# Kernel optimization log

Hardware: AMD Instinct MI355X
Metric: run time of the kernel (lower is better)

The kernel has to match this reference:

```python
import jax, jax.numpy as jnp
import numpy as np

B, S, E, H = 2, 2048, 2048, 16
D = E // H  # head_dim = 128


def setup_inputs() -> dict:
    key = jax.random.key(0)
    ks = jax.random.split(key, 7)
    x = jax.random.normal(ks[0], (B, S, E), dtype=jnp.float32)
    cos = jax.random.uniform(ks[1], (S, D), dtype=jnp.float32)
    sin = jax.random.uniform(ks[2], (S, D), dtype=jnp.float32)
    scale = 1.0 / np.sqrt(E)
    Wq = jax.random.normal(ks[3], (E, E), dtype=jnp.float32) * scale
    Wk = jax.random.normal(ks[4], (E, E), dtype=jnp.float32) * scale
    Wv = jax.random.normal(ks[5], (E, E), dtype=jnp.float32) * scale
    Wo = jax.random.normal(ks[6], (E, E), dtype=jnp.float32) * scale
    return {"x": x, "cos": cos, "sin": sin, "Wq": Wq, "Wk": Wk, "Wv": Wv, "Wo": Wo}


def _apply_rope(t, cos, sin):
    # t: [B, S, H, D]; cos/sin: [S, D]. NeoX rotate-half.
    half = t.shape[-1] // 2
    rotate = jnp.concatenate([-t[..., half:], t[..., :half]], axis=-1)
    return t * cos[None, :, None, :] + rotate * sin[None, :, None, :]


def reference(x, cos, sin, Wq, Wk, Wv, Wo):
    b, s, e = x.shape
    q = (x @ Wq.T).reshape(b, s, H, D)
    k = (x @ Wk.T).reshape(b, s, H, D)
    v = (x @ Wv.T).reshape(b, s, H, D)
    q = _apply_rope(q, cos, sin).transpose(0, 2, 1, 3)  # [B,H,S,D]
    k = _apply_rope(k, cos, sin).transpose(0, 2, 1, 3)
    v = v.transpose(0, 2, 1, 3)
    scale = 1.0 / jnp.sqrt(jnp.asarray(D, dtype=x.dtype))
    scores = jnp.einsum("bhqd,bhkd->bhqk", q, k) * scale
    causal = jnp.tril(jnp.ones((s, s), dtype=bool))
    scores = jnp.where(causal[None, None], scores, jnp.asarray(-1e30, dtype=scores.dtype))
    attn = jax.nn.softmax(scores, axis=-1)
    out = jnp.einsum("bhqk,bhkd->bhqd", attn, v)  # [B,H,S,D]
    out = out.transpose(0, 2, 1, 3).reshape(b, s, e)
    return out @ Wo.T
```

## Files before the change

### kernel.cpp

```cpp
#include <hip/hip_runtime.h>
#include <stdint.h>

typedef unsigned short u16;
typedef __attribute__((ext_vector_type(8))) short short8;
typedef __attribute__((ext_vector_type(4))) float f32x4;
typedef __attribute__((ext_vector_type(16))) float f32x16;

#define B_ 2
#define S_ 2048
#define E_ 2048
#define H_ 16
#define D_ 128
#define M_ 4096

__device__ __forceinline__ u16 f2bf(float f) {
  unsigned u = __float_as_uint(f);
  u = u + 0x7FFFu + ((u >> 16) & 1u);
  return (u16)(u >> 16);
}
__device__ __forceinline__ float bf2f(u16 h) {
  return __uint_as_float(((unsigned)h) << 16);
}

#define GLD16(gp, lp) __builtin_amdgcn_global_load_lds(                      \
    (__attribute__((address_space(1))) void*)(gp),                           \
    (__attribute__((address_space(3))) void*)(lp), 16, 0, 0)

__global__ void cast_bf16(const float4* __restrict__ src, ushort4* __restrict__ dst, int n4) {
  int i = blockIdx.x * 256 + threadIdx.x;
  if (i < n4) {
    float4 v = src[i];
    ushort4 o;
    o.x = f2bf(v.x); o.y = f2bf(v.y); o.z = f2bf(v.z); o.w = f2bf(v.w);
    dst[i] = o;
  }
}

__global__ void cast4_bf16(const float4* __restrict__ w0, const float4* __restrict__ w1,
                           const float4* __restrict__ w2, const float4* __restrict__ w3,
                           ushort4* __restrict__ o0, ushort4* __restrict__ o1,
                           ushort4* __restrict__ o2, ushort4* __restrict__ o3, int n4) {
  const int i = blockIdx.x * 256 + threadIdx.x;
  if (i >= n4) return;
  const float4* s; ushort4* d;
  switch (blockIdx.y) {
    case 0: s = w0; d = o0; break;
    case 1: s = w1; d = o1; break;
    case 2: s = w2; d = o2; break;
    default: s = w3; d = o3; break;
  }
  float4 v = s[i];
  ushort4 o;
  o.x = f2bf(v.x); o.y = f2bf(v.y); o.z = f2bf(v.z); o.w = f2bf(v.w);
  d[i] = o;
}

template <int MODE>
__launch_bounds__(512, 1)
__global__ void gemm256(const u16* __restrict__ A, const u16* __restrict__ Bw,
                        void* __restrict__ Cp, int M, int N, int K, int bxpx,
                        const float* __restrict__ cosT, const float* __restrict__ sinT) {
  __shared__ alignas(16) u16 SMEM[73728];
  u16* const LA = SMEM;
  u16* const LB = SMEM + 24576;
  const int tid = threadIdx.x, wave = tid >> 6, lane = tid & 63;
  const int xcd = blockIdx.x & 7;
  const int j = blockIdx.x >> 3;
  const int bx = xcd * bxpx + (j % bxpx);
  const int by = j / bxpx;
  const int m0 = by * 128, n0 = bx * 256;
  const int wm = (wave >> 2) * 64, wn = (wave & 3) * 64;
  const int lrow = lane & 15, lq = lane >> 4;

  auto stage0 = [&](int buf, int kt) {
    const int k0 = kt * 64;
#pragma unroll
    for (int i = 0; i < 2; ++i) {
      const int c = i * 512 + tid;
      const int row = c >> 3, k = c & 7;
      GLD16(A + (size_t)(m0 + row) * K + k0 + ((k ^ (row & 7)) * 8),
            LA + buf * 8192 + i * 4096 + wave * 512);
    }
    {
      const int c = tid;
      const int row = c >> 3, k = c & 7;
      GLD16(Bw + (size_t)(n0 + row) * K + k0 + ((k ^ (row & 7)) * 8),
            LB + buf * 16384 + wave * 512);
    }
  };
  auto stage1 = [&](int buf, int kt) {
    const int k0 = kt * 64;
#pragma unroll
    for (int i = 1; i < 4; ++i) {
      const int c = i * 512 + tid;
      const int row = c >> 3, k = c & 7;
      GLD16(Bw + (size_t)(n0 + row) * K + k0 + ((k ^ (row & 7)) * 8),
            LB + buf * 16384 + i * 4096 + wave * 512);
    }
  };

  f32x4 acc[4][4] = {};
  const int NT = K >> 6;
  stage0(0, 0); stage1(0, 0);
  stage0(1, 1); stage1(1, 1);
  asm volatile("s_waitcnt vmcnt(6) lgkmcnt(0)" ::: "memory");
  __builtin_amdgcn_sched_barrier(0);
  __builtin_amdgcn_s_barrier();

  for (int t = 0; t < NT; ++t) {
    const int cur = t % 3;
    const int sb = (t + 2) % 3;
    const bool dostage = (t + 2) < NT;

    short8 a0[4], b0[4];
#pragma unroll
    for (int m = 0; m < 4; ++m) {
      const int row = wm + m * 16 + lrow;
      a0[m] = *(const short8*)&LA[cur * 8192 + row * 64 + ((lq ^ (row & 7)) * 8)];
    }
#pragma unroll
    for (int n = 0; n < 4; ++n) {
      const int row = wn + n * 16 + lrow;
      b0[n] = *(const short8*)&LB[cur * 16384 + row * 64 + ((lq ^ (row & 7)) * 8)];
    }
    if (dostage) stage0(sb, t + 2);
    __builtin_amdgcn_sched_barrier(0);
    __builtin_amdgcn_s_barrier();
    __builtin_amdgcn_sched_barrier(0);
    __builtin_amdgcn_s_setprio(1);
#pragma unroll
    for (int m = 0; m < 4; ++m)
#pragma unroll
      for (int n = 0; n < 4; ++n)
        acc[m][n] = __builtin_amdgcn_mfma_f32_16x16x32_bf16(a0[m], b0[n], acc[m][n], 0, 0, 0);
    __builtin_amdgcn_s_setprio(0);

    short8 a1[4], b1[4];
#pragma unroll
    for (int m = 0; m < 4; ++m) {
      const int row = wm + m * 16 + lrow;
      a1[m] = *(const short8*)&LA[cur * 8192 + row * 64 + (((4 + lq) ^ (row & 7)) * 8)];
    }
#pragma unroll
    for (int n = 0; n < 4; ++n) {
      const int row = wn + n * 16 + lrow;
      b1[n] = *(const short8*)&LB[cur * 16384 + row * 64 + (((4 + lq) ^ (row & 7)) * 8)];
    }
    if (dostage) stage1(sb, t + 2);
    if (t < NT - 2) { asm volatile("s_waitcnt vmcnt(6) lgkmcnt(0)" ::: "memory"); }
    else            { asm volatile("s_waitcnt vmcnt(0) lgkmcnt(0)" ::: "memory"); }
    __builtin_amdgcn_sched_barrier(0);
    __builtin_amdgcn_s_barrier();
    __builtin_amdgcn_sched_barrier(0);
    __builtin_amdgcn_s_setprio(1);
#pragma unroll
    for (int m = 0; m < 4; ++m)
#pragma unroll
      for (int n = 0; n < 4; ++n)
        acc[m][n] = __builtin_amdgcn_mfma_f32_16x16x32_bf16(a1[m], b1[n], acc[m][n], 0, 0, 0);
    __builtin_amdgcn_s_setprio(0);
  }

  const int rbase = lq * 4;
  if (MODE == 1) {
#pragma unroll
    for (int m = 0; m < 4; ++m)
#pragma unroll
      for (int n = 0; n < 4; ++n)
#pragma unroll
        for (int r = 0; r < 4; ++r) {
          const int mm = m0 + wm + m * 16 + rbase + r;
          const int nn = n0 + wn + n * 16 + lrow;
          ((float*)Cp)[(size_t)mm * N + nn] = acc[m][n][r];
        }
    return;
  }

  u16* ct = SMEM;
#pragma unroll
  for (int m = 0; m < 4; ++m)
#pragma unroll
    for (int n = 0; n < 4; ++n)
#pragma unroll
      for (int r = 0; r < 4; ++r)
        ct[(wm + m * 16 + rbase + r) * 272 + wn + n * 16 + lrow] = f2bf(acc[m][n][r]);
  __syncthreads();

  const int tz = n0 >> 11;
  const int bb = m0 >> 11, s0 = m0 & (S_ - 1);
  const int h0 = (n0 >> 7) & 15;
  const size_t NXc = (size_t)B_ * S_ * E_;
  u16* dst = (u16*)Cp + (size_t)tz * NXc;

  if (tz < 2) {
    const float sc = (tz == 0) ? 0.12751744154f : 1.f;
#pragma unroll
    for (int i = 0; i < 8; ++i) {
      const int idx = i * 512 + tid;
      const int row = idx >> 5, c8 = (idx & 31) * 8;
      const int head = c8 >> 7, hd = c8 & 127;
      const int s = s0 + row;
      short8 self = *(const short8*)&ct[row * 272 + c8];
      short8 part = *(const short8*)&ct[row * 272 + (c8 ^ 64)];
      float4 cv0 = *(const float4*)&cosT[s * D_ + hd];
      float4 cv1 = *(const float4*)&cosT[s * D_ + hd + 4];
      float4 sv0 = *(const float4*)&sinT[s * D_ + hd];
      float4 sv1 = *(const float4*)&sinT[s * D_ + hd + 4];
      float cv[8] = {cv0.x, cv0.y, cv0.z, cv0.w, cv1.x, cv1.y, cv1.z, cv1.w};
      float sv[8] = {sv0.x, sv0.y, sv0.z, sv0.w, sv1.x, sv1.y, sv1.z, sv1.w};
      short8 o;
      if (hd < 64) {
#pragma unroll
        for (int jj = 0; jj < 8; ++jj) {
          const float x1 = bf2f((u16)self[jj]), x2 = bf2f((u16)part[jj]);
          o[jj] = (short)f2bf((x1 * cv[jj] - x2 * sv[jj]) * sc);
        }
      } else {
#pragma unroll
        for (int jj = 0; jj < 8; ++jj) {
          const float x2 = bf2f((u16)self[jj]), x1 = bf2f((u16)part[jj]);
          o[jj] = (short)f2bf((x2 * cv[jj] + x1 * sv[jj]) * sc);
        }
      }
      *(short8*)&dst[(((size_t)bb * H_ + h0 + head) * S_ + s) * D_ + hd] = o;
    }
  } else {
#pragma unroll
    for (int i = 0; i < 8; ++i) {
      const int task = i * 512 + tid;
      const int dcol = task & 255, sch = task >> 8;
      short8 v;
#pragma unroll
      for (int jj = 0; jj < 8; ++jj) v[jj] = ct[(sch * 8 + jj) * 272 + dcol];
      const int h = h0 + (dcol >> 7), hd = dcol & 127;
      *(short8*)&dst[(((size_t)bb * H_ + h) * D_ + hd) * S_ + s0 + sch * 8] = v;
    }
  }
}

__launch_bounds__(512, 2)
__global__ void attn_fwd(const u16* __restrict__ Q, const u16* __restrict__ Kt,
                         const u16* __restrict__ VT, u16* __restrict__ Out) {
  __shared__ alignas(16) u16 SB[2][2][16384];
  __shared__ float MLB[4][64][2];
  const int tid = threadIdx.x, wave = tid >> 6, lane = tid & 63;
  const int hw = blockIdx.x;
  const int lid = (hw & 7) * 32 + (hw >> 3);
  const int p = lid & 7, bh = lid >> 3;
  const int bb = bh >> 4, h = bh & 15;
  const u16* Qh = Q + (size_t)bh * S_ * D_;
  const u16* Kh = Kt + (size_t)bh * S_ * D_;
  const u16* Vh = VT + (size_t)bh * D_ * S_;
  const int grp = wave >> 2, w4 = wave & 3;
  const int l31 = lane & 31, hi = lane >> 5;

  auto stage = [&](int buf, int kv0) {
#pragma unroll
    for (int pp = 0; pp < 4; ++pp) {
      const int g = pp * 4 + w4;
      const int c = g * 64 + lane;
      const int srow = c >> 4, dch = c & 15;
      GLD16(Kh + (size_t)(kv0 + srow) * D_ + ((dch ^ (srow & 7)) * 8), &SB[grp][buf][g * 512]);
      const int drow = c >> 3, sch = c & 7;
      GLD16(Vh + (size_t)drow * S_ + kv0 + ((sch ^ (drow & 7)) * 8), &SB[grp][buf][8192 + g * 512]);
    }
  };

  float* obuf = (float*)&SB[1][0][0];

  const int qts[2] = {15 - p, p};
#pragma unroll 1
  for (int seg = 0; seg < 2; ++seg) {
    const int t = qts[seg];
    const int iters = t + 1;
    const int q0 = t * 128 + w4 * 32;
    const int qg = q0 + l31;

    short8 qf[8];
#pragma unroll
    for (int m = 0; m < 8; ++m)
      qf[m] = *(const short8*)&Qh[(size_t)qg * D_ + m * 16 + hi * 8];

    f32x16 od[4] = {};
    float mr = 0.f, lsum = 0.f;

    stage(0, grp * 64);
    int cur = 0;

    for (int i = 0; i < iters; ++i) {
      __syncthreads();
      if (i + 1 < iters) stage(cur ^ 1, (2 * (i + 1) + grp) * 64);
      const int kv0 = (2 * i + grp) * 64;
      const u16* Kc = &SB[grp][cur][0];
      const u16* Vc = &SB[grp][cur][8192];

      f32x16 s0 = {}, s1 = {};
      __builtin_amdgcn_s_setprio(1);
#pragma unroll
      for (int m = 0; m < 8; ++m) {
        const int col = m * 16 + hi * 8;
        const int sw = (l31 & 7) << 3;
        short8 k0 = *(const short8*)&Kc[l31 * 128 + (col ^ sw)];
        short8 k1 = *(const short8*)&Kc[(32 + l31) * 128 + (col ^ sw)];
        s0 = __builtin_amdgcn_mfma_f32_32x32x16_bf16(k0, qf[m], s0, 0, 0, 0);
        s1 = __builtin_amdgcn_mfma_f32_32x32x16_bf16(k1, qf[m], s1, 0, 0, 0);
      }
      __builtin_amdgcn_s_setprio(0);

      if (kv0 + 63 > q0) {
#pragma unroll
        for (int r = 0; r < 16; ++r) {
          const int k0g = kv0 + (r & 3) + 8 * (r >> 2) + 4 * hi;
          if (k0g > qg)      s0[r] = -1e30f;
          if (k0g + 32 > qg) s1[r] = -1e30f;
        }
      }

      float mloc = s0[0];
#pragma unroll
      for (int r = 1; r < 16; ++r) mloc = fmaxf(mloc, s0[r]);
#pragma unroll
      for (int r = 0; r < 16; ++r) mloc = fmaxf(mloc, s1[r]);
      const float mx = fmaxf(mloc, __shfl_xor(mloc, 32));
      const bool need = !__all(mx <= mr + 8.f);
      float corr = 1.f;
      if (need) {
        const float mnew = fmaxf(mr, mx);
        corr = exp2f(mr - mnew);
        mr = mnew;
      }
      float sloc = 0.f;
#pragma unroll
      for (int r = 0; r < 16; ++r) { s0[r] = exp2f(s0[r] - mr); sloc += s0[r]; }
#pragma unroll
      for (int r = 0; r < 16; ++r) { s1[r] = exp2f(s1[r] - mr); sloc += s1[r]; }
      const float rsum = sloc + __shfl_xor(sloc, 32);
      lsum = lsum * corr + rsum;
      if (need) {
#pragma unroll
        for (int dt = 0; dt < 4; ++dt)
#pragma unroll
          for (int r = 0; r < 16; ++r) od[dt][r] *= corr;
      }

      unsigned W0[4][2], W1[4][2];
#pragma unroll
      for (int c = 0; c < 4; ++c)
#pragma unroll
        for (int pr = 0; pr < 2; ++pr) {
          asm("v_cvt_pk_bf16_f32 %0, %1, %2"
              : "=v"(W0[c][pr]) : "v"(s0[4 * c + 2 * pr]), "v"(s0[4 * c + 2 * pr + 1]));
          asm("v_cvt_pk_bf16_f32 %0, %1, %2"
              : "=v"(W1[c][pr]) : "v"(s1[4 * c + 2 * pr]), "v"(s1[4 * c + 2 * pr + 1]));
        }

      __builtin_amdgcn_s_setprio(1);
#pragma unroll
      for (int kk = 0; kk < 4; ++kk) {
        const int cown = 2 * (kk & 1) + hi, csend = 2 * (kk & 1) + 1 - hi;
        unsigned o0, o1, sd0, sd1;
        if (kk < 2) { o0 = W0[cown][0]; o1 = W0[cown][1]; sd0 = W0[csend][0]; sd1 = W0[csend][1]; }
        else        { o0 = W1[cown][0]; o1 = W1[cown][1]; sd0 = W1[csend][0]; sd1 = W1[csend][1]; }
        const unsigned r0 = (unsigned)__shfl_xor((int)sd0, 32);
        const unsigned r1 = (unsigned)__shfl_xor((int)sd1, 32);
        uint4 bw;
        if (hi == 0) bw = make_uint4(o0, o1, r0, r1);
        else         bw = make_uint4(r0, r1, o0, o1);
        const short8 pf = *(const short8*)&bw;
        const int slot = 2 * kk + hi;
#pragma unroll
        for (int dt = 0; dt < 4; ++dt) {
          const int row = dt * 32 + l31;
          const short8 vf = *(const short8*)&Vc[row * 64 + ((slot ^ (row & 7)) * 8)];
          od[dt] = __builtin_amdgcn_mfma_f32_32x32x16_bf16(vf, pf, od[dt], 0, 0, 0);
        }
      }
      __builtin_amdgcn_s_setprio(0);
      cur ^= 1;
    }

    __syncthreads();
    if (grp == 1) {
      MLB[w4][lane][0] = mr;
      MLB[w4][lane][1] = lsum;
#pragma unroll
      for (int dt = 0; dt < 4; ++dt)
#pragma unroll
        for (int r = 0; r < 16; ++r)
          obuf[(dt * 16 + r) * 256 + w4 * 64 + lane] = od[dt][r];
    }
    __syncthreads();
    if (grp == 0) {
      const float mB = MLB[w4][lane][0];
      const float lB = MLB[w4][lane][1];
      const float m = fmaxf(mr, mB);
      const float aA = exp2f(mr - m), aB = exp2f(mB - m);
      lsum = lsum * aA + lB * aB;
#pragma unroll
      for (int dt = 0; dt < 4; ++dt)
#pragma unroll
        for (int r = 0; r < 16; ++r)
          od[dt][r] = od[dt][r] * aA + obuf[(dt * 16 + r) * 256 + w4 * 64 + lane] * aB;

      const float inv = 1.f / lsum;
      const size_t obase = ((size_t)bb * S_ + qg) * E_ + h * D_;
#pragma unroll
      for (int dt = 0; dt < 4; ++dt)
#pragma unroll
        for (int g = 0; g < 4; ++g) {
          ushort4 w;
          w.x = f2bf(od[dt][4 * g + 0] * inv);
          w.y = f2bf(od[dt][4 * g + 1] * inv);
          w.z = f2bf(od[dt][4 * g + 2] * inv);
          w.w = f2bf(od[dt][4 * g + 3] * inv);
          *(ushort4*)&Out[obase + dt * 32 + 8 * g + 4 * hi] = w;
        }
    }
    __syncthreads();
  }
}

extern "C" void kernel_launch(void* const* d_in, const int* in_sizes, int n_in,
                              void* d_out, int out_size, void* d_ws, size_t ws_size,
                              hipStream_t stream) {
  const float* x    = (const float*)d_in[0];
  const float* cosT = (const float*)d_in[1];
  const float* sinT = (const float*)d_in[2];
  const float* Wq   = (const float*)d_in[3];
  const float* Wk   = (const float*)d_in[4];
  const float* Wv   = (const float*)d_in[5];
  const float* Wo   = (const float*)d_in[6];
  float* out = (float*)d_out;

  const size_t NX = (size_t)B_ * S_ * E_;
  const size_t NW = (size_t)E_ * E_;
  u16* ws  = (u16*)d_ws;
  u16* xb  = ws;
  u16* Wqb = xb + NX;
  u16* Wkb = Wqb + NW;
  u16* Wvb = Wkb + NW;
  u16* Wob = Wvb + NW;
  u16* Qb  = Wob + NW;
  u16* Kb  = Qb + NX;
  u16* VTb = Kb + NX;
  u16* Ab  = VTb + NX;

  cast_bf16<<<(int)(NX / 4 / 256), 256, 0, stream>>>((const float4*)x, (ushort4*)xb, (int)(NX / 4));
  cast4_bf16<<<dim3((int)(NW / 4 / 256), 4), 256, 0, stream>>>(
      (const float4*)Wq, (const float4*)Wk, (const float4*)Wv, (const float4*)Wo,
      (ushort4*)Wqb, (ushort4*)Wkb, (ushort4*)Wvb, (ushort4*)Wob, (int)(NW / 4));

  gemm256<0><<<dim3(768), 512, 0, stream>>>(xb, Wqb, Qb, M_, 3 * E_, E_, 3, cosT, sinT);

  attn_fwd<<<dim3(256), 512, 0, stream>>>(Qb, Kb, VTb, Ab);

  gemm256<1><<<dim3(256), 512, 0, stream>>>(Ab, Wob, out, M_, E_, E_, 1, nullptr, nullptr);
}
```

Measured before the change: 249.0 us.

## Pre-swizzle weights into MFMA fragment layout and load B directly to registers

The weight cast kernel now transposes each weight into a fragment-major bf16 layout through shared memory, so every wave can read its B operand straight from global memory into registers with contiguous 16-byte loads. The GEMM drops the LDS staging for B, shrinks shared memory, and double-buffers B fragments in registers while A stays in a triple-buffered LDS pipeline. The loop now has one barrier per K-tile instead of two. In exchange it raises register pressure and global load traffic per wave, since B tiles are no longer shared across the two row-waves through LDS, and it makes the cast kernel more complex.

Result: slower. 269.5 us (+8.3%).

```diff
diff --git a/kernel.cpp b/kernel.cpp
--- a/kernel.cpp
+++ b/kernel.cpp
@@ -36,23 +36,43 @@
   }
 }
 
-__global__ void cast4_bf16(const float4* __restrict__ w0, const float4* __restrict__ w1,
-                           const float4* __restrict__ w2, const float4* __restrict__ w3,
-                           ushort4* __restrict__ o0, ushort4* __restrict__ o1,
-                           ushort4* __restrict__ o2, ushort4* __restrict__ o3, int n4) {
-  const int i = blockIdx.x * 256 + threadIdx.x;
-  if (i >= n4) return;
-  const float4* s; ushort4* d;
+__global__ void cast4t(const float* __restrict__ w0, const float* __restrict__ w1,
+                       const float* __restrict__ w2, const float* __restrict__ w3,
+                       u16* __restrict__ o0, u16* __restrict__ o1,
+                       u16* __restrict__ o2, u16* __restrict__ o3) {
+  __shared__ float ls[16][521];
+  const int tid = threadIdx.x;
+  const float* s; u16* d;
   switch (blockIdx.y) {
     case 0: s = w0; d = o0; break;
     case 1: s = w1; d = o1; break;
     case 2: s = w2; d = o2; break;
     default: s = w3; d = o3; break;
   }
-  float4 v = s[i];
-  ushort4 o;
-  o.x = f2bf(v.x); o.y = f2bf(v.y); o.z = f2bf(v.z); o.w = f2bf(v.w);
-  d[i] = o;
+  const int K = E_, K32 = K >> 5;
+  const int p = blockIdx.x >> 2;
+  const int kb = blockIdx.x & 3;
+#pragma unroll
+  for (int i = 0; i < 8; ++i) {
+    const int task = i * 256 + tid;
+    const int r = task >> 7, c4 = task & 127;
+    float4 v = *(const float4*)&s[(size_t)(p * 16 + r) * K + kb * 512 + c4 * 4];
+    ls[r][c4 * 4 + 0] = v.x; ls[r][c4 * 4 + 1] = v.y;
+    ls[r][c4 * 4 + 2] = v.z; ls[r][c4 * 4 + 3] = v.w;
+  }
+  __syncthreads();
+#pragma unroll
+  for (int i = 0; i < 4; ++i) {
+    const int task = i * 256 + tid;
+    const int kc_l = task >> 6, l = task & 63;
+    const int ko = l >> 4, rr = l & 15;
+    short8 o;
+#pragma unroll
+    for (int e = 0; e < 8; ++e)
+      o[e] = (short)f2bf(ls[rr][kc_l * 32 + ko * 8 + e]);
+    const int kc = kb * 16 + kc_l;
+    *(short8*)&d[((size_t)(p * K32 + kc) * 64 + l) * 8] = o;
+  }
 }
 
 template <int MODE>
@@ -60,9 +80,8 @@
 __global__ void gemm256(const u16* __restrict__ A, const u16* __restrict__ Bw,
                         void* __restrict__ Cp, int M, int N, int K, int bxpx,
                         const float* __restrict__ cosT, const float* __restrict__ sinT) {
-  __shared__ alignas(16) u16 SMEM[73728];
+  __shared__ alignas(16) u16 SMEM[34816];
   u16* const LA = SMEM;
-  u16* const LB = SMEM + 24576;
   const int tid = threadIdx.x, wave = tid >> 6, lane = tid & 63;
   const int xcd = blockIdx.x & 7;
   const int j = blockIdx.x >> 3;
@@ -71,8 +90,10 @@
   const int m0 = by * 128, n0 = bx * 256;
   const int wm = (wave >> 2) * 64, wn = (wave & 3) * 64;
   const int lrow = lane & 15, lq = lane >> 4;
-
-  auto stage0 = [&](int buf, int kt) {
+  const int K32 = K >> 5;
+  const int pn0 = (n0 + wn) >> 4;
+
+  auto stageA = [&](int buf, int kt) {
     const int k0 = kt * 64;
 #pragma unroll
     for (int i = 0; i < 2; ++i) {
@@ -81,84 +102,54 @@
       GLD16(A + (size_t)(m0 + row) * K + k0 + ((k ^ (row & 7)) * 8),
             LA + buf * 8192 + i * 4096 + wave * 512);
     }
-    {
-      const int c = tid;
-      const int row = c >> 3, k = c & 7;
-      GLD16(Bw + (size_t)(n0 + row) * K + k0 + ((k ^ (row & 7)) * 8),
-            LB + buf * 16384 + wave * 512);
-    }
   };
-  auto stage1 = [&](int buf, int kt) {
-    const int k0 = kt * 64;
-#pragma unroll
-    for (int i = 1; i < 4; ++i) {
-      const int c = i * 512 + tid;
-      const int row = c >> 3, k = c & 7;
-      GLD16(Bw + (size_t)(n0 + row) * K + k0 + ((k ^ (row & 7)) * 8),
-            LB + buf * 16384 + i * 4096 + wave * 512);
-    }
+  auto loadB = [&](short8 (&dst)[2][4], int kt) {
+    const int kc = kt * 2;
+#pragma unroll
+    for (int ch = 0; ch < 2; ++ch)
+#pragma unroll
+      for (int n = 0; n < 4; ++n)
+        dst[ch][n] = *(const short8*)&Bw[((size_t)(pn0 + n) * K32 + kc + ch) * 512 + lane * 8];
   };
 
   f32x4 acc[4][4] = {};
+  short8 b0[2][4], b1[2][4];
   const int NT = K >> 6;
-  stage0(0, 0); stage1(0, 0);
-  stage0(1, 1); stage1(1, 1);
-  asm volatile("s_waitcnt vmcnt(6) lgkmcnt(0)" ::: "memory");
+  stageA(0, 0); stageA(1, 1);
+  loadB(b0, 0);
+  asm volatile("s_waitcnt vmcnt(10)" ::: "memory");
   __builtin_amdgcn_sched_barrier(0);
   __builtin_amdgcn_s_barrier();
-
-  for (int t = 0; t < NT; ++t) {
-    const int cur = t % 3;
-    const int sb = (t + 2) % 3;
-    const bool dostage = (t + 2) < NT;
-
-    short8 a0[4], b0[4];
-#pragma unroll
-    for (int m = 0; m < 4; ++m) {
-      const int row = wm + m * 16 + lrow;
-      a0[m] = *(const short8*)&LA[cur * 8192 + row * 64 + ((lq ^ (row & 7)) * 8)];
-    }
-#pragma unroll
-    for (int n = 0; n < 4; ++n) {
-      const int row = wn + n * 16 + lrow;
-      b0[n] = *(const short8*)&LB[cur * 16384 + row * 64 + ((lq ^ (row & 7)) * 8)];
-    }
-    if (dostage) stage0(sb, t + 2);
+  __builtin_amdgcn_sched_barrier(0);
+
+  auto body = [&](int t, short8 (&bc)[2][4], short8 (&bn)[2][4]) {
+    const int cur = t % 3, sb = (t + 2) % 3;
+    if (t + 2 < NT) stageA(sb, t + 2);
+    if (t + 1 < NT) loadB(bn, t + 1);
+    short8 a[2][4];
+#pragma unroll
+    for (int ch = 0; ch < 2; ++ch)
+#pragma unroll
+      for (int m = 0; m < 4; ++m) {
+        const int row = wm + m * 16 + lrow;
+        a[ch][m] = *(const short8*)&LA[cur * 8192 + row * 64 + (((ch * 4 + lq) ^ (row & 7)) * 8)];
+      }
+    __builtin_amdgcn_s_setprio(1);
+#pragma unroll
+    for (int ch = 0; ch < 2; ++ch)
+#pragma unroll
+      for (int m = 0; m < 4; ++m)
+#pragma unroll
+        for (int n = 0; n < 4; ++n)
+          acc[m][n] = __builtin_amdgcn_mfma_f32_16x16x32_bf16(a[ch][m], bc[ch][n], acc[m][n], 0, 0, 0);
+    __builtin_amdgcn_s_setprio(0);
     __builtin_amdgcn_sched_barrier(0);
     __builtin_amdgcn_s_barrier();
     __builtin_amdgcn_sched_barrier(0);
-    __builtin_amdgcn_s_setprio(1);
-#pragma unroll
-    for (int m = 0; m < 4; ++m)
-#pragma unroll
-      for (int n = 0; n < 4; ++n)
-        acc[m][n] = __builtin_amdgcn_mfma_f32_16x16x32_bf16(a0[m], b0[n], acc[m][n], 0, 0, 0);
-    __builtin_amdgcn_s_setprio(0);
-
-    short8 a1[4], b1[4];
-#pragma unroll
-    for (int m = 0; m < 4; ++m) {
-      const int row = wm + m * 16 + lrow;
-      a1[m] = *(const short8*)&LA[cur * 8192 + row * 64 + (((4 + lq) ^ (row & 7)) * 8)];
-    }
-#pragma unroll
-    for (int n = 0; n < 4; ++n) {
-      const int row = wn + n * 16 + lrow;
-      b1[n] = *(const short8*)&LB[cur * 16384 + row * 64 + (((4 + lq) ^ (row & 7)) * 8)];
-    }
-    if (dostage) stage1(sb, t + 2);
-    if (t < NT - 2) { asm volatile("s_waitcnt vmcnt(6) lgkmcnt(0)" ::: "memory"); }
-    else            { asm volatile("s_waitcnt vmcnt(0) lgkmcnt(0)" ::: "memory"); }
-    __builtin_amdgcn_sched_barrier(0);
-    __builtin_amdgcn_s_barrier();
-    __builtin_amdgcn_sched_barrier(0);
-    __builtin_amdgcn_s_setprio(1);
-#pragma unroll
-    for (int m = 0; m < 4; ++m)
-#pragma unroll
-      for (int n = 0; n < 4; ++n)
-        acc[m][n] = __builtin_amdgcn_mfma_f32_16x16x32_bf16(a1[m], b1[n], acc[m][n], 0, 0, 0);
-    __builtin_amdgcn_s_setprio(0);
+  };
+  for (int t = 0; t < NT; t += 2) {
+    body(t, b0, b1);
+    body(t + 1, b1, b0);
   }
 
   const int rbase = lq * 4;
@@ -446,9 +437,7 @@
   u16* Ab  = VTb + NX;
 
   cast_bf16<<<(int)(NX / 4 / 256), 256, 0, stream>>>((const float4*)x, (ushort4*)xb, (int)(NX / 4));
-  cast4_bf16<<<dim3((int)(NW / 4 / 256), 4), 256, 0, stream>>>(
-      (const float4*)Wq, (const float4*)Wk, (const float4*)Wv, (const float4*)Wo,
-      (ushort4*)Wqb, (ushort4*)Wkb, (ushort4*)Wvb, (ushort4*)Wob, (int)(NW / 4));
+  cast4t<<<dim3(512, 4), 256, 0, stream>>>(Wq, Wk, Wv, Wo, Wqb, Wkb, Wvb, Wob);
 
   gemm256<0><<<dim3(768), 512, 0, stream>>>(xb, Wqb, Qb, M_, 3 * E_, E_, 3, cosT, sinT);
 
```

## Split attention KV loop across four wave groups with tree merge

Applied to the files above, without the earlier changes.

The attention kernel moves from two to four KV-split wave groups per block (1024 threads), each handling 32-key chunks instead of 64. Partial softmax states are then merged in two stages through shared memory. The aim is more independent waves per block and shorter per-wave dependency chains to hide latency. In exchange each MFMA batch is smaller, there are more barriers and merge passes, and launch bounds drop the per-SM occupancy hint, which may raise register pressure.

Result: slower. 361.5 us (+45.2%).

```diff
diff --git a/kernel.cpp b/kernel.cpp
--- a/kernel.cpp
+++ b/kernel.cpp
@@ -238,12 +238,13 @@
   }
 }
 
-__launch_bounds__(512, 2)
+__launch_bounds__(1024)
 __global__ void attn_fwd(const u16* __restrict__ Q, const u16* __restrict__ Kt,
                          const u16* __restrict__ VT, u16* __restrict__ Out) {
-  __shared__ alignas(16) u16 SB[2][2][16384];
-  __shared__ float MLB[4][64][2];
+  __shared__ alignas(16) u16 SB[4][2][8192];
+  __shared__ float MLB[3][4][64][2];
   const int tid = threadIdx.x, wave = tid >> 6, lane = tid & 63;
+  const int grp = wave >> 2, w4 = wave & 3;
   const int hw = blockIdx.x;
   const int lid = (hw & 7) * 32 + (hw >> 3);
   const int p = lid & 7, bh = lid >> 3;
@@ -251,22 +252,22 @@
   const u16* Qh = Q + (size_t)bh * S_ * D_;
   const u16* Kh = Kt + (size_t)bh * S_ * D_;
   const u16* Vh = VT + (size_t)bh * D_ * S_;
-  const int grp = wave >> 2, w4 = wave & 3;
   const int l31 = lane & 31, hi = lane >> 5;
 
   auto stage = [&](int buf, int kv0) {
 #pragma unroll
-    for (int pp = 0; pp < 4; ++pp) {
+    for (int pp = 0; pp < 2; ++pp) {
       const int g = pp * 4 + w4;
       const int c = g * 64 + lane;
       const int srow = c >> 4, dch = c & 15;
       GLD16(Kh + (size_t)(kv0 + srow) * D_ + ((dch ^ (srow & 7)) * 8), &SB[grp][buf][g * 512]);
-      const int drow = c >> 3, sch = c & 7;
-      GLD16(Vh + (size_t)drow * S_ + kv0 + ((sch ^ (drow & 7)) * 8), &SB[grp][buf][8192 + g * 512]);
+      const int drow = c >> 2, sch = c & 3;
+      GLD16(Vh + (size_t)drow * S_ + kv0 + ((sch ^ (drow & 3)) * 8), &SB[grp][buf][4096 + g * 512]);
     }
   };
 
-  float* obuf = (float*)&SB[1][0][0];
+  float* obufA = (float*)&SB[0][0][0];
+  float* obufB = obufA + 16384;
 
   const int qts[2] = {15 - p, p};
 #pragma unroll 1
@@ -284,43 +285,40 @@
     f32x16 od[4] = {};
     float mr = 0.f, lsum = 0.f;
 
-    stage(0, grp * 64);
+    stage(0, grp * 32);
     int cur = 0;
 
     for (int i = 0; i < iters; ++i) {
       __syncthreads();
-      if (i + 1 < iters) stage(cur ^ 1, (2 * (i + 1) + grp) * 64);
-      const int kv0 = (2 * i + grp) * 64;
+      if (i + 1 < iters) stage(cur ^ 1, ((i + 1) * 4 + grp) * 32);
+      const int kv0 = (i * 4 + grp) * 32;
       const u16* Kc = &SB[grp][cur][0];
-      const u16* Vc = &SB[grp][cur][8192];
-
-      f32x16 s0 = {}, s1 = {};
+      const u16* Vc = &SB[grp][cur][4096];
+
+      f32x16 s0 = {};
       __builtin_amdgcn_s_setprio(1);
 #pragma unroll
       for (int m = 0; m < 8; ++m) {
         const int col = m * 16 + hi * 8;
-        const int sw = (l31 & 7) << 3;
-        short8 k0 = *(const short8*)&Kc[l31 * 128 + (col ^ sw)];
-        short8 k1 = *(const short8*)&Kc[(32 + l31) * 128 + (col ^ sw)];
+        short8 k0 = *(const short8*)&Kc[l31 * 128 + (col ^ ((l31 & 7) << 3))];
         s0 = __builtin_amdgcn_mfma_f32_32x32x16_bf16(k0, qf[m], s0, 0, 0, 0);
-        s1 = __builtin_amdgcn_mfma_f32_32x32x16_bf16(k1, qf[m], s1, 0, 0, 0);
       }
       __builtin_amdgcn_s_setprio(0);
 
-      if (kv0 + 63 > q0) {
+      if (kv0 + 31 > q0) {
 #pragma unroll
         for (int r = 0; r < 16; ++r) {
-          const int k0g = kv0 + (r & 3) + 8 * (r >> 2) + 4 * hi;
-          if (k0g > qg)      s0[r] = -1e30f;
-          if (k0g + 32 > qg) s1[r] = -1e30f;
-        }
-      }
-
-      float mloc = s0[0];
-#pragma unroll
-      for (int r = 1; r < 16; ++r) mloc = fmaxf(mloc, s0[r]);
-#pragma unroll
-      for (int r = 0; r < 16; ++r) mloc = fmaxf(mloc, s1[r]);
+          const int kg = kv0 + (r & 3) + 8 * (r >> 2) + 4 * hi;
+          if (kg > qg) s0[r] = -1e30f;
+        }
+      }
+
+      float m0 = fmaxf(s0[0], s0[1]), m1 = fmaxf(s0[2], s0[3]);
+      float m2 = fmaxf(s0[4], s0[5]), m3 = fmaxf(s0[6], s0[7]);
+      float m4 = fmaxf(s0[8], s0[9]), m5 = fmaxf(s0[10], s0[11]);
+      float m6 = fmaxf(s0[12], s0[13]), m7 = fmaxf(s0[14], s0[15]);
+      float mloc = fmaxf(fmaxf(fmaxf(m0, m1), fmaxf(m2, m3)),
+                         fmaxf(fmaxf(m4, m5), fmaxf(m6, m7)));
       const float mx = fmaxf(mloc, __shfl_xor(mloc, 32));
       const bool need = !__all(mx <= mr + 8.f);
       float corr = 1.f;
@@ -332,8 +330,6 @@
       float sloc = 0.f;
 #pragma unroll
       for (int r = 0; r < 16; ++r) { s0[r] = exp2f(s0[r] - mr); sloc += s0[r]; }
-#pragma unroll
-      for (int r = 0; r < 16; ++r) { s1[r] = exp2f(s1[r] - mr); sloc += s1[r]; }
       const float rsum = sloc + __shfl_xor(sloc, 32);
       lsum = lsum * corr + rsum;
       if (need) {
@@ -343,26 +339,21 @@
           for (int r = 0; r < 16; ++r) od[dt][r] *= corr;
       }
 
-      unsigned W0[4][2], W1[4][2];
+      unsigned W0[4][2];
 #pragma unroll
       for (int c = 0; c < 4; ++c)
 #pragma unroll
-        for (int pr = 0; pr < 2; ++pr) {
+        for (int pr = 0; pr < 2; ++pr)
           asm("v_cvt_pk_bf16_f32 %0, %1, %2"
               : "=v"(W0[c][pr]) : "v"(s0[4 * c + 2 * pr]), "v"(s0[4 * c + 2 * pr + 1]));
-          asm("v_cvt_pk_bf16_f32 %0, %1, %2"
-              : "=v"(W1[c][pr]) : "v"(s1[4 * c + 2 * pr]), "v"(s1[4 * c + 2 * pr + 1]));
-        }
 
       __builtin_amdgcn_s_setprio(1);
 #pragma unroll
-      for (int kk = 0; kk < 4; ++kk) {
-        const int cown = 2 * (kk & 1) + hi, csend = 2 * (kk & 1) + 1 - hi;
-        unsigned o0, o1, sd0, sd1;
-        if (kk < 2) { o0 = W0[cown][0]; o1 = W0[cown][1]; sd0 = W0[csend][0]; sd1 = W0[csend][1]; }
-        else        { o0 = W1[cown][0]; o1 = W1[cown][1]; sd0 = W1[csend][0]; sd1 = W1[csend][1]; }
-        const unsigned r0 = (unsigned)__shfl_xor((int)sd0, 32);
-        const unsigned r1 = (unsigned)__shfl_xor((int)sd1, 32);
+      for (int kk = 0; kk < 2; ++kk) {
+        const int cown = 2 * kk + hi, csend = 2 * kk + 1 - hi;
+        const unsigned o0 = W0[cown][0], o1 = W0[cown][1];
+        const unsigned r0 = (unsigned)__shfl_xor((int)W0[csend][0], 32);
+        const unsigned r1 = (unsigned)__shfl_xor((int)W0[csend][1], 32);
         uint4 bw;
         if (hi == 0) bw = make_uint4(o0, o1, r0, r1);
         else         bw = make_uint4(r0, r1, o0, o1);
@@ -371,7 +362,7 @@
 #pragma unroll
         for (int dt = 0; dt < 4; ++dt) {
           const int row = dt * 32 + l31;
-          const short8 vf = *(const short8*)&Vc[row * 64 + ((slot ^ (row & 7)) * 8)];
+          const short8 vf = *(const short8*)&Vc[row * 32 + ((slot ^ (row & 3)) * 8)];
           od[dt] = __builtin_amdgcn_mfma_f32_32x32x16_bf16(vf, pf, od[dt], 0, 0, 0);
         }
       }
@@ -380,27 +371,53 @@
     }
 
     __syncthreads();
-    if (grp == 1) {
-      MLB[w4][lane][0] = mr;
-      MLB[w4][lane][1] = lsum;
+    if (grp == 1 || grp == 3) {
+      float* ob = (grp == 1) ? obufA : obufB;
+      MLB[grp - 1][w4][lane][0] = mr;
+      MLB[grp - 1][w4][lane][1] = lsum;
 #pragma unroll
       for (int dt = 0; dt < 4; ++dt)
 #pragma unroll
         for (int r = 0; r < 16; ++r)
-          obuf[(dt * 16 + r) * 256 + w4 * 64 + lane] = od[dt][r];
+          ob[(dt * 16 + r) * 256 + w4 * 64 + lane] = od[dt][r];
     }
     __syncthreads();
-    if (grp == 0) {
-      const float mB = MLB[w4][lane][0];
-      const float lB = MLB[w4][lane][1];
+    if (grp == 0 || grp == 2) {
+      const float* ob = (grp == 0) ? obufA : obufB;
+      const float mB = MLB[grp][w4][lane][0];
+      const float lB = MLB[grp][w4][lane][1];
       const float m = fmaxf(mr, mB);
       const float aA = exp2f(mr - m), aB = exp2f(mB - m);
       lsum = lsum * aA + lB * aB;
+      mr = m;
 #pragma unroll
       for (int dt = 0; dt < 4; ++dt)
 #pragma unroll
         for (int r = 0; r < 16; ++r)
-          od[dt][r] = od[dt][r] * aA + obuf[(dt * 16 + r) * 256 + w4 * 64 + lane] * aB;
+          od[dt][r] = od[dt][r] * aA + ob[(dt * 16 + r) * 256 + w4 * 64 + lane] * aB;
+    }
+    __syncthreads();
+    if (grp == 2) {
+      MLB[1][w4][lane][0] = mr;
+      MLB[1][w4][lane][1] = lsum;
+#pragma unroll
+      for (int dt = 0; dt < 4; ++dt)
+#pragma unroll
+        for (int r = 0; r < 16; ++r)
+          obufA[(dt * 16 + r) * 256 + w4 * 64 + lane] = od[dt][r];
+    }
+    __syncthreads();
+    if (grp == 0) {
+      const float mB = MLB[1][w4][lane][0];
+      const float lB = MLB[1][w4][lane][1];
+      const float m = fmaxf(mr, mB);
+      const float aA = exp2f(mr - m), aB = exp2f(mB - m);
+      lsum = lsum * aA + lB * aB;
+#pragma unroll
+      for (int dt = 0; dt < 4; ++dt)
+#pragma unroll
+        for (int r = 0; r < 16; ++r)
+          od[dt][r] = od[dt][r] * aA + obufA[(dt * 16 + r) * 256 + w4 * 64 + lane] * aB;
 
       const float inv = 1.f / lsum;
       const size_t obase = ((size_t)bb * S_ + qg) * E_ + h * D_;
@@ -452,7 +469,7 @@
 
   gemm256<0><<<dim3(768), 512, 0, stream>>>(xb, Wqb, Qb, M_, 3 * E_, E_, 3, cosT, sinT);
 
-  attn_fwd<<<dim3(256), 512, 0, stream>>>(Qb, Kb, VTb, Ab);
+  attn_fwd<<<dim3(256), 1024, 0, stream>>>(Qb, Kb, VTb, Ab);
 
   gemm256<1><<<dim3(256), 512, 0, stream>>>(Ab, Wob, out, M_, E_, E_, 1, nullptr, nullptr);
 }
```

## Halve GEMM K-tile and LDS footprint to fit two blocks per CU

Applied to the files above, without the earlier changes.

The projection GEMM's K-step drops from 64 to 32. The triple-buffered LDS shrinks by half, so launch bounds can request two 512-thread blocks per CU. The two half-step load and MFMA phases per iteration merge into one, with a single barrier and a smaller waitcnt, and a __syncthreads now guards reuse of LDS in the epilogue. The attention kernel's launch bound drops to one block per CU, which loosens its register limit, since its LDS use already allows only one block. The trade-off is more loop iterations and barriers per K, and register pressure from the doubled GEMM occupancy.

New measurement: 249.6 us. No clear change (+0.2%).

```diff
diff --git a/kernel.cpp b/kernel.cpp
--- a/kernel.cpp
+++ b/kernel.cpp
@@ -56,13 +56,13 @@
 }
 
 template <int MODE>
-__launch_bounds__(512, 1)
+__launch_bounds__(512, 2)
 __global__ void gemm256(const u16* __restrict__ A, const u16* __restrict__ Bw,
                         void* __restrict__ Cp, int M, int N, int K, int bxpx,
                         const float* __restrict__ cosT, const float* __restrict__ sinT) {
-  __shared__ alignas(16) u16 SMEM[73728];
+  __shared__ alignas(16) u16 SMEM[36864];
   u16* const LA = SMEM;
-  u16* const LB = SMEM + 24576;
+  u16* const LB = SMEM + 12288;
   const int tid = threadIdx.x, wave = tid >> 6, lane = tid & 63;
   const int xcd = blockIdx.x & 7;
   const int j = blockIdx.x >> 3;
@@ -72,82 +72,47 @@
   const int wm = (wave >> 2) * 64, wn = (wave & 3) * 64;
   const int lrow = lane & 15, lq = lane >> 4;
 
-  auto stage0 = [&](int buf, int kt) {
-    const int k0 = kt * 64;
+  auto stage = [&](int buf, int kt) {
+    const int k0 = kt * 32;
+    {
+      const int c = tid;
+      const int row = c >> 2, k = c & 3;
+      GLD16(A + (size_t)(m0 + row) * K + k0 + ((k ^ (row & 3)) * 8),
+            LA + buf * 4096 + wave * 512);
+    }
 #pragma unroll
     for (int i = 0; i < 2; ++i) {
       const int c = i * 512 + tid;
-      const int row = c >> 3, k = c & 7;
-      GLD16(A + (size_t)(m0 + row) * K + k0 + ((k ^ (row & 7)) * 8),
-            LA + buf * 8192 + i * 4096 + wave * 512);
-    }
-    {
-      const int c = tid;
-      const int row = c >> 3, k = c & 7;
-      GLD16(Bw + (size_t)(n0 + row) * K + k0 + ((k ^ (row & 7)) * 8),
-            LB + buf * 16384 + wave * 512);
+      const int row = c >> 2, k = c & 3;
+      GLD16(Bw + (size_t)(n0 + row) * K + k0 + ((k ^ (row & 3)) * 8),
+            LB + buf * 8192 + i * 4096 + wave * 512);
     }
   };
-  auto stage1 = [&](int buf, int kt) {
-    const int k0 = kt * 64;
-#pragma unroll
-    for (int i = 1; i < 4; ++i) {
-      const int c = i * 512 + tid;
-      const int row = c >> 3, k = c & 7;
-      GLD16(Bw + (size_t)(n0 + row) * K + k0 + ((k ^ (row & 7)) * 8),
-            LB + buf * 16384 + i * 4096 + wave * 512);
-    }
-  };
 
   f32x4 acc[4][4] = {};
-  const int NT = K >> 6;
-  stage0(0, 0); stage1(0, 0);
-  stage0(1, 1); stage1(1, 1);
-  asm volatile("s_waitcnt vmcnt(6) lgkmcnt(0)" ::: "memory");
+  const int NT = K >> 5;
+  stage(0, 0); stage(1, 1);
+  asm volatile("s_waitcnt vmcnt(3) lgkmcnt(0)" ::: "memory");
   __builtin_amdgcn_sched_barrier(0);
   __builtin_amdgcn_s_barrier();
 
   for (int t = 0; t < NT; ++t) {
     const int cur = t % 3;
     const int sb = (t + 2) % 3;
-    const bool dostage = (t + 2) < NT;
-
-    short8 a0[4], b0[4];
+
+    short8 a[4], b[4];
 #pragma unroll
     for (int m = 0; m < 4; ++m) {
       const int row = wm + m * 16 + lrow;
-      a0[m] = *(const short8*)&LA[cur * 8192 + row * 64 + ((lq ^ (row & 7)) * 8)];
+      a[m] = *(const short8*)&LA[cur * 4096 + row * 32 + ((lq ^ (row & 3)) * 8)];
     }
 #pragma unroll
     for (int n = 0; n < 4; ++n) {
       const int row = wn + n * 16 + lrow;
-      b0[n] = *(const short8*)&LB[cur * 16384 + row * 64 + ((lq ^ (row & 7)) * 8)];
-    }
-    if (dostage) stage0(sb, t + 2);
-    __builtin_amdgcn_sched_barrier(0);
-    __builtin_amdgcn_s_barrier();
-    __builtin_amdgcn_sched_barrier(0);
-    __builtin_amdgcn_s_setprio(1);
-#pragma unroll
-    for (int m = 0; m < 4; ++m)
-#pragma unroll
-      for (int n = 0; n < 4; ++n)
-        acc[m][n] = __builtin_amdgcn_mfma_f32_16x16x32_bf16(a0[m], b0[n], acc[m][n], 0, 0, 0);
-    __builtin_amdgcn_s_setprio(0);
-
-    short8 a1[4], b1[4];
-#pragma unroll
-    for (int m = 0; m < 4; ++m) {
-      const int row = wm + m * 16 + lrow;
-      a1[m] = *(const short8*)&LA[cur * 8192 + row * 64 + (((4 + lq) ^ (row & 7)) * 8)];
-    }
-#pragma unroll
-    for (int n = 0; n < 4; ++n) {
-      const int row = wn + n * 16 + lrow;
-      b1[n] = *(const short8*)&LB[cur * 16384 + row * 64 + (((4 + lq) ^ (row & 7)) * 8)];
-    }
-    if (dostage) stage1(sb, t + 2);
-    if (t < NT - 2) { asm volatile("s_waitcnt vmcnt(6) lgkmcnt(0)" ::: "memory"); }
+      b[n] = *(const short8*)&LB[cur * 8192 + row * 32 + ((lq ^ (row & 3)) * 8)];
+    }
+    if (t + 2 < NT) stage(sb, t + 2);
+    if (t < NT - 2) { asm volatile("s_waitcnt vmcnt(3) lgkmcnt(0)" ::: "memory"); }
     else            { asm volatile("s_waitcnt vmcnt(0) lgkmcnt(0)" ::: "memory"); }
     __builtin_amdgcn_sched_barrier(0);
     __builtin_amdgcn_s_barrier();
@@ -157,7 +122,7 @@
     for (int m = 0; m < 4; ++m)
 #pragma unroll
       for (int n = 0; n < 4; ++n)
-        acc[m][n] = __builtin_amdgcn_mfma_f32_16x16x32_bf16(a1[m], b1[n], acc[m][n], 0, 0, 0);
+        acc[m][n] = __builtin_amdgcn_mfma_f32_16x16x32_bf16(a[m], b[n], acc[m][n], 0, 0, 0);
     __builtin_amdgcn_s_setprio(0);
   }
 
@@ -176,6 +141,7 @@
     return;
   }
 
+  __syncthreads();
   u16* ct = SMEM;
 #pragma unroll
   for (int m = 0; m < 4; ++m)
@@ -238,7 +204,7 @@
   }
 }
 
-__launch_bounds__(512, 2)
+__launch_bounds__(512, 1)
 __global__ void attn_fwd(const u16* __restrict__ Q, const u16* __restrict__ Kt,
                          const u16* __restrict__ VT, u16* __restrict__ Out) {
   __shared__ alignas(16) u16 SB[2][2][16384];
```
